# Kernel optimization log

Measured on AMD Instinct MI355X. Metric: run time of the kernel, lower is better.

The kernel has to match this reference:

```python
import jax, jax.numpy as jnp
import numpy as np

B, C, L = 2, 256, 2048   # batch, emb_dim, seq_len
D, H = 64, 8             # d_model (per-head), n_heads
HD = D * H
EPS = 1e-8


def glob_ln(x, gamma, beta):
    # x: (B, C, L); normalize over all non-batch dims, affine over channel dim 1
    mean = jnp.mean(x, axis=(1, 2), keepdims=True)
    var = jnp.mean((x - mean) ** 2, axis=(1, 2), keepdims=True)
    normed = (x - mean) / jnp.sqrt(var + EPS)
    return gamma[None, :, None] * normed + beta[None, :, None]


def pos_encoding(length, dim):
    pos = jnp.arange(length, dtype=jnp.float32)[:, None]
    div = jnp.exp(jnp.arange(0, dim, 2, dtype=jnp.float32) * (-np.log(10000.0) / dim))
    ang = pos * div  # (L, dim/2)
    return jnp.stack([jnp.sin(ang), jnp.cos(ang)], axis=-1).reshape(length, dim)


def setup_inputs() -> dict:
    key = jax.random.key(0)
    ks = jax.random.split(key, 16)
    s_in = 1.0 / np.sqrt(C)
    s_hd = 1.0 / np.sqrt(HD)
    return {
        "x": jax.random.normal(ks[0], (B, C, L), dtype=jnp.float32),
        "Wq": jax.random.uniform(ks[1], (HD, C), minval=-s_in, maxval=s_in),
        "bq": jax.random.uniform(ks[2], (HD,), minval=-s_in, maxval=s_in),
        "Wk": jax.random.uniform(ks[3], (HD, C), minval=-s_in, maxval=s_in),
        "bk": jax.random.uniform(ks[4], (HD,), minval=-s_in, maxval=s_in),
        "Wv": jax.random.uniform(ks[5], (HD, C), minval=-s_in, maxval=s_in),
        "bv": jax.random.uniform(ks[6], (HD,), minval=-s_in, maxval=s_in),
        "Wo": jax.random.uniform(ks[7], (C, HD), minval=-s_hd, maxval=s_hd),
        "bo": jax.random.uniform(ks[8], (C,), minval=-s_hd, maxval=s_hd),
        "g_mha": jnp.ones((C,)), "b_mha": jnp.zeros((C,)),
        "conv_w": jax.random.uniform(ks[9], (C, C), minval=-s_in, maxval=s_in),
        "conv_b": jax.random.uniform(ks[10], (C,), minval=-s_in, maxval=s_in),
        "g_ffn": jnp.ones((C,)), "b_ffn": jnp.zeros((C,)),
        "alpha": jnp.float32(0.25),
        "g_out": jnp.ones((C,)), "b_out": jnp.zeros((C,)),
    }


def reference(x, Wq, bq, Wk, bk, Wv, bv, Wo, bo, g_mha, b_mha,
              conv_w, conv_b, g_ffn, b_ffn, alpha, g_out, b_out):
    scale = 1.0 / np.sqrt(D)
    t = jnp.transpose(x, (0, 2, 1))            # (B, L, C)
    t = t + pos_encoding(L, C)[None]
    # multi-head attention (self)
    q = (scale * (t @ Wq.T + bq)).reshape(B, L, H, D)
    k = (t @ Wk.T + bk).reshape(B, L, H, D)
    v = (t @ Wv.T + bv).reshape(B, L, H, D)
    scores = jnp.einsum('nlhd,nshd->nhls', q, k)  # (B, H, L, L)
    attn = jax.nn.softmax(scores, axis=-1)
    o = jnp.einsum('nhls,nshd->nlhd', attn, v).reshape(B, L, HD)
    t = t + (o @ Wo.T + bo)                    # residual
    y = glob_ln(jnp.transpose(t, (0, 2, 1)), g_mha, b_mha)  # (B, C, L)
    # FFN: 1x1 conv + GlobLN + PReLU
    f = jnp.einsum('bcl,oc->bol', y, conv_w) + conv_b[None, :, None]
    f = glob_ln(f, g_ffn, b_ffn)
    f = jnp.where(f >= 0, f, alpha * f)
    return glob_ln(f + y, g_out, b_out)
```

## Files before the change

### kernel.cpp

```cpp
#include <hip/hip_runtime.h>
#include <hip/hip_bf16.h>
#include <math.h>

#define BB   2
#define CC   256
#define LL   2048
#define DD   64
#define HH   8
#define HDIM 512
#define BLQ  (BB*LL)
#define EPSV 1e-8f

typedef __attribute__((ext_vector_type(8))) short short8;
typedef __attribute__((ext_vector_type(4))) float f32x4;

__device__ __forceinline__ float wred_sum(float v) {
#pragma unroll
    for (int off = 32; off > 0; off >>= 1) v += __shfl_down(v, off, 64);
    return v;
}
__device__ __forceinline__ unsigned short f2bf(float x) {
    union { float f; unsigned u; } a; a.f = x;
    unsigned r = a.u + 0x7fff + ((a.u >> 16) & 1);
    return (unsigned short)(r >> 16);
}
__device__ __forceinline__ unsigned pk(float a, float b) {
    return (unsigned)f2bf(a) | ((unsigned)f2bf(b) << 16);
}
__device__ __forceinline__ short8 ld_frag(const unsigned short* p) {
    union { short8 v; uint2 u[2]; } f;
    f.u[0] = *(const uint2*)p;
    f.u[1] = *(const uint2*)(p + 4);
    return f.v;
}

__global__ __launch_bounds__(256) void k_prep(const float* __restrict__ x,
                                              float* __restrict__ t,
                                              unsigned short* __restrict__ tb) {
    __shared__ float tr[64][65];
    int l0 = blockIdx.x * 64, c0 = blockIdx.y * 64, b = blockIdx.z;
    int tid = threadIdx.x, r = tid >> 2, q = tid & 3;
#pragma unroll
    for (int p = 0; p < 4; ++p) {
        int lc = 4 * (q + 4 * p);
        float4 v = *(const float4*)&x[((size_t)(b * CC + c0 + r)) * LL + l0 + lc];
        tr[lc + 0][r] = v.x; tr[lc + 1][r] = v.y; tr[lc + 2][r] = v.z; tr[lc + 3][r] = v.w;
    }
    __syncthreads();
    int lg = l0 + r;
#pragma unroll
    for (int p = 0; p < 4; ++p) {
        int cc = 4 * (q + 4 * p);
        float4 v = *(const float4*)&tr[r][cc];
        float pe[4];
#pragma unroll
        for (int i = 0; i < 4; ++i) {
            int cg = c0 + cc + i;
            float freq = __expf((float)(cg & ~1) * (-9.210340371976184f / (float)CC));
            float ang = (float)lg * freq;
            pe[i] = (cg & 1) ? __cosf(ang) : __sinf(ang);
        }
        v.x += pe[0]; v.y += pe[1]; v.z += pe[2]; v.w += pe[3];
        size_t o = ((size_t)(b * LL + lg)) * CC + c0 + cc;
        *(float4*)&t[o] = v;
        uint2 u; u.x = pk(v.x, v.y); u.y = pk(v.z, v.w);
        *(uint2*)&tb[o] = u;
    }
}

__global__ __launch_bounds__(256) void k_cvtw(const float* __restrict__ Wq, const float* __restrict__ Wk,
                                              const float* __restrict__ Wv, const float* __restrict__ Wo,
                                              const float* __restrict__ Wc,
                                              unsigned short* __restrict__ dqkv,
                                              unsigned short* __restrict__ dWo,
                                              unsigned short* __restrict__ dWc) {
    int idx = (blockIdx.x * 256 + threadIdx.x) * 4;
    const float* s; unsigned short* d;
    if (idx < 131072)      { s = Wq + idx;          d = dqkv + idx; }
    else if (idx < 262144) { s = Wk + idx - 131072; d = dqkv + idx; }
    else if (idx < 393216) { s = Wv + idx - 262144; d = dqkv + idx; }
    else if (idx < 524288) { s = Wo + idx - 393216; d = dWo + idx - 393216; }
    else                   { s = Wc + idx - 524288; d = dWc + idx - 524288; }
    float4 v = *(const float4*)s;
    uint2 u; u.x = pk(v.x, v.y); u.y = pk(v.z, v.w);
    *(uint2*)d = u;
}

#define MLDK 68
__global__ __launch_bounds__(256) void k_mm(const unsigned short* __restrict__ A,
                                            const unsigned short* __restrict__ W,
                                            const float* __restrict__ b0,
                                            const float* __restrict__ b1,
                                            const float* __restrict__ b2,
                                            const float* resid,
                                            float* out, unsigned short* outb,
                                            float* pstat,
                                            int mode, int M, int N, int K) {
    __shared__ unsigned short As[2][64][MLDK];
    __shared__ unsigned short Ws[2][64][MLDK];
    __shared__ float rs[4][2];
    int tid = threadIdx.x;
    int w = tid >> 6, lane = tid & 63, g = lane >> 4, qi = lane & 15;
    int bm = blockIdx.x * 64, bn = blockIdx.y * 64;
    int wr = w >> 1, wc = w & 1;
    int srow = tid >> 2, sq = tid & 3;
    bool vseg = (mode == 1) && (bn >= 1024);
    f32x4 acc[2][2];
    acc[0][0] = acc[0][1] = acc[1][0] = acc[1][1] = (f32x4){0.f, 0.f, 0.f, 0.f};
    uint4 ra[2], rw[2];
#pragma unroll
    for (int p = 0; p < 2; ++p) {
        ra[p] = *(const uint4*)&A[(size_t)(bm + srow) * K + (sq + 4 * p) * 8];
        rw[p] = *(const uint4*)&W[(size_t)(bn + srow) * K + (sq + 4 * p) * 8];
    }
    int nt = K >> 6;
    for (int it = 0; it < nt; ++it) {
        int buf = it & 1;
#pragma unroll
        for (int p = 0; p < 2; ++p) {
            *(uint2*)&As[buf][srow][(sq + 4 * p) * 8]     = make_uint2(ra[p].x, ra[p].y);
            *(uint2*)&As[buf][srow][(sq + 4 * p) * 8 + 4] = make_uint2(ra[p].z, ra[p].w);
            *(uint2*)&Ws[buf][srow][(sq + 4 * p) * 8]     = make_uint2(rw[p].x, rw[p].y);
            *(uint2*)&Ws[buf][srow][(sq + 4 * p) * 8 + 4] = make_uint2(rw[p].z, rw[p].w);
        }
        __syncthreads();
        if (it + 1 < nt) {
            int k0 = (it + 1) << 6;
#pragma unroll
            for (int p = 0; p < 2; ++p) {
                ra[p] = *(const uint4*)&A[(size_t)(bm + srow) * K + k0 + (sq + 4 * p) * 8];
                rw[p] = *(const uint4*)&W[(size_t)(bn + srow) * K + k0 + (sq + 4 * p) * 8];
            }
        }
#pragma unroll
        for (int c = 0; c < 2; ++c) {
            short8 wf0 = ld_frag(&Ws[buf][wr * 32 + 0  + qi][c * 32 + 8 * g]);
            short8 wf1 = ld_frag(&Ws[buf][wr * 32 + 16 + qi][c * 32 + 8 * g]);
            short8 af0 = ld_frag(&As[buf][wc * 32 + 0  + qi][c * 32 + 8 * g]);
            short8 af1 = ld_frag(&As[buf][wc * 32 + 16 + qi][c * 32 + 8 * g]);
            if (!vseg) {
                acc[0][0] = __builtin_amdgcn_mfma_f32_16x16x32_bf16(wf0, af0, acc[0][0], 0, 0, 0);
                acc[0][1] = __builtin_amdgcn_mfma_f32_16x16x32_bf16(wf0, af1, acc[0][1], 0, 0, 0);
                acc[1][0] = __builtin_amdgcn_mfma_f32_16x16x32_bf16(wf1, af0, acc[1][0], 0, 0, 0);
                acc[1][1] = __builtin_amdgcn_mfma_f32_16x16x32_bf16(wf1, af1, acc[1][1], 0, 0, 0);
            } else {
                acc[0][0] = __builtin_amdgcn_mfma_f32_16x16x32_bf16(af0, wf0, acc[0][0], 0, 0, 0);
                acc[0][1] = __builtin_amdgcn_mfma_f32_16x16x32_bf16(af0, wf1, acc[0][1], 0, 0, 0);
                acc[1][0] = __builtin_amdgcn_mfma_f32_16x16x32_bf16(af1, wf0, acc[1][0], 0, 0, 0);
                acc[1][1] = __builtin_amdgcn_mfma_f32_16x16x32_bf16(af1, wf1, acc[1][1], 0, 0, 0);
            }
        }
    }
    if (mode == 0) {
        float s = 0.f, s2 = 0.f;
#pragma unroll
        for (int fi = 0; fi < 2; ++fi)
#pragma unroll
            for (int fj = 0; fj < 2; ++fj) {
                int n0 = bn + wr * 32 + fi * 16 + 4 * g;
                int m  = bm + wc * 32 + fj * 16 + qi;
                float4 bi = *(const float4*)&b0[n0];
                float4 v;
                v.x = acc[fi][fj][0] + bi.x; v.y = acc[fi][fj][1] + bi.y;
                v.z = acc[fi][fj][2] + bi.z; v.w = acc[fi][fj][3] + bi.w;
                if (resid) {
                    float4 rv = *(const float4*)&resid[(size_t)m * N + n0];
                    v.x += rv.x; v.y += rv.y; v.z += rv.z; v.w += rv.w;
                }
                *(float4*)&out[(size_t)m * N + n0] = v;
                s  += (v.x + v.y) + (v.z + v.w);
                s2 += v.x * v.x + v.y * v.y + v.z * v.z + v.w * v.w;
            }
        if (pstat) {
            s = wred_sum(s); s2 = wred_sum(s2);
            if (lane == 0) { rs[w][0] = s; rs[w][1] = s2; }
            __syncthreads();
            if (tid == 0) {
                int bid = blockIdx.y * gridDim.x + blockIdx.x;
                pstat[bid * 2 + 0] = rs[0][0] + rs[1][0] + rs[2][0] + rs[3][0];
                pstat[bid * 2 + 1] = rs[0][1] + rs[1][1] + rs[2][1] + rs[3][1];
            }
        }
    } else if (!vseg) {
        int seg = bn >> 9;
        const float* bs = seg ? b1 : b0;
        float sc = seg ? 1.f : 0.125f;
#pragma unroll
        for (int fi = 0; fi < 2; ++fi)
#pragma unroll
            for (int fj = 0; fj < 2; ++fj) {
                int nn0 = (bn & 511) + wr * 32 + fi * 16 + 4 * g;
                int m   = bm + wc * 32 + fj * 16 + qi;
                int b = m >> 11, l = m & (LL - 1);
                int h = nn0 >> 6, d0 = nn0 & 63;
                float4 bi = *(const float4*)&bs[nn0];
                uint2 u;
                u.x = pk(sc * (acc[fi][fj][0] + bi.x), sc * (acc[fi][fj][1] + bi.y));
                u.y = pk(sc * (acc[fi][fj][2] + bi.z), sc * (acc[fi][fj][3] + bi.w));
                *(uint2*)&outb[(size_t)seg * 2097152 +
                               (((size_t)(b * HH + h)) * LL + l) * DD + d0] = u;
            }
    } else {
#pragma unroll
        for (int fi = 0; fi < 2; ++fi)
#pragma unroll
            for (int fj = 0; fj < 2; ++fj) {
                int m0 = bm + wc * 32 + fi * 16 + 4 * g;
                int nn = (bn & 511) + wr * 32 + fj * 16 + qi;
                int b = m0 >> 11, l0 = m0 & (LL - 1);
                int h = nn >> 6, d = nn & 63;
                float bi = b2[nn];
                uint2 u;
                u.x = pk(acc[fi][fj][0] + bi, acc[fi][fj][1] + bi);
                u.y = pk(acc[fi][fj][2] + bi, acc[fi][fj][3] + bi);
                *(uint2*)&outb[(size_t)2 * 2097152 +
                               (((size_t)(b * HH + h)) * DD + d) * LL + l0] = u;
            }
    }
}

#define LDK 68
__global__ __launch_bounds__(256) void k_attn(const unsigned short* __restrict__ QKV,
                                              unsigned short* __restrict__ o) {
    int h = blockIdx.y, b = blockIdx.z;
    int tid = threadIdx.x;
    int w = tid >> 6, lane = tid & 63, g = lane >> 4, qi = lane & 15;
    int q0 = blockIdx.x * 64 + w * 16;
    __shared__ unsigned short Ks[2][64][LDK];
    __shared__ unsigned short Vts[2][64][LDK];
    __shared__ unsigned short Pw[4][16][LDK];
    const size_t bh = (size_t)(b * HH + h);
    const unsigned short* Qg = QKV + bh * LL * DD;
    const unsigned short* Kg = QKV + 2097152 + bh * LL * DD;
    const unsigned short* Vg = QKV + (size_t)2 * 2097152 + bh * DD * LL;

    short8 qf[2];
#pragma unroll
    for (int c = 0; c < 2; ++c)
        qf[c] = *(const short8*)&Qg[(size_t)(q0 + qi) * DD + c * 32 + 8 * g];

    f32x4 ot[4];
#pragma unroll
    for (int db = 0; db < 4; ++db) ot[db] = (f32x4){0.f, 0.f, 0.f, 0.f};
    float m = -INFINITY, sum = 0.f;

    int srow = tid >> 2, sq = tid & 3;
    uint4 kr[2], vr[2];
#pragma unroll
    for (int p = 0; p < 2; ++p) {
        kr[p] = *(const uint4*)&Kg[(size_t)srow * DD + (sq + 4 * p) * 8];
        vr[p] = *(const uint4*)&Vg[(size_t)srow * LL + (sq + 4 * p) * 8];
    }
    for (int it = 0; it < LL / 64; ++it) {
        int buf = it & 1;
#pragma unroll
        for (int p = 0; p < 2; ++p) {
            *(uint2*)&Ks[buf][srow][(sq + 4 * p) * 8]      = make_uint2(kr[p].x, kr[p].y);
            *(uint2*)&Ks[buf][srow][(sq + 4 * p) * 8 + 4]  = make_uint2(kr[p].z, kr[p].w);
            *(uint2*)&Vts[buf][srow][(sq + 4 * p) * 8]     = make_uint2(vr[p].x, vr[p].y);
            *(uint2*)&Vts[buf][srow][(sq + 4 * p) * 8 + 4] = make_uint2(vr[p].z, vr[p].w);
        }
        __syncthreads();
        if (it + 1 < LL / 64) {
            int s1 = (it + 1) * 64;
#pragma unroll
            for (int p = 0; p < 2; ++p) {
                kr[p] = *(const uint4*)&Kg[(size_t)(s1 + srow) * DD + (sq + 4 * p) * 8];
                vr[p] = *(const uint4*)&Vg[(size_t)srow * LL + s1 + (sq + 4 * p) * 8];
            }
        }
        f32x4 st[4];
        __builtin_amdgcn_s_setprio(1);
#pragma unroll
        for (int sb = 0; sb < 4; ++sb) {
            f32x4 a = (f32x4){0.f, 0.f, 0.f, 0.f};
#pragma unroll
            for (int c = 0; c < 2; ++c) {
                short8 kf = ld_frag(&Ks[buf][sb * 16 + qi][c * 32 + 8 * g]);
                a = __builtin_amdgcn_mfma_f32_16x16x32_bf16(kf, qf[c], a, 0, 0, 0);
            }
            st[sb] = a;
        }
        __builtin_amdgcn_s_setprio(0);
        float tmax = -INFINITY;
#pragma unroll
        for (int sb = 0; sb < 4; ++sb)
#pragma unroll
            for (int r = 0; r < 4; ++r) tmax = fmaxf(tmax, st[sb][r]);
        tmax = fmaxf(tmax, __shfl_xor(tmax, 16, 64));
        tmax = fmaxf(tmax, __shfl_xor(tmax, 32, 64));
        if (!__all(tmax - m <= 8.f)) {
            float mnew = fmaxf(m, tmax);
            float corr = __expf(m - mnew);
            m = mnew;
            sum *= corr;
#pragma unroll
            for (int db = 0; db < 4; ++db)
#pragma unroll
                for (int r = 0; r < 4; ++r) ot[db][r] *= corr;
        }
        float ps = 0.f;
#pragma unroll
        for (int sb = 0; sb < 4; ++sb) {
            float p0 = __expf(st[sb][0] - m);
            float p1 = __expf(st[sb][1] - m);
            float p2 = __expf(st[sb][2] - m);
            float p3 = __expf(st[sb][3] - m);
            ps += (p0 + p1) + (p2 + p3);
            uint2 w2; w2.x = pk(p0, p1); w2.y = pk(p2, p3);
            *(uint2*)&Pw[w][qi][sb * 16 + 4 * g] = w2;
        }
        sum += ps;
        __builtin_amdgcn_s_setprio(1);
#pragma unroll
        for (int db = 0; db < 4; ++db)
#pragma unroll
            for (int sc = 0; sc < 2; ++sc) {
                short8 vf = ld_frag(&Vts[buf][db * 16 + qi][sc * 32 + 8 * g]);
                short8 pf = ld_frag(&Pw[w][qi][sc * 32 + 8 * g]);
                ot[db] = __builtin_amdgcn_mfma_f32_16x16x32_bf16(vf, pf, ot[db], 0, 0, 0);
            }
        __builtin_amdgcn_s_setprio(0);
    }
    sum += __shfl_xor(sum, 16, 64);
    sum += __shfl_xor(sum, 32, 64);
    float rinv = 1.f / sum;
#pragma unroll
    for (int db = 0; db < 4; ++db) {
        int d0 = db * 16 + 4 * g;
        uint2 u;
        u.x = pk(ot[db][0] * rinv, ot[db][1] * rinv);
        u.y = pk(ot[db][2] * rinv, ot[db][3] * rinv);
        *(uint2*)&o[((size_t)(b * LL + q0 + qi)) * HDIM + h * DD + d0] = u;
    }
}

__global__ __launch_bounds__(256) void k_ln(const float* in,
                                            const float* __restrict__ g,
                                            const float* __restrict__ be,
                                            const float* __restrict__ pin,
                                            const float* __restrict__ add,
                                            const float* __restrict__ alpha_ptr,
                                            float* out, unsigned short* outb,
                                            float* pout) {
    __shared__ float rs[4][2];
    int tid = threadIdx.x;
    int b = blockIdx.x >> 9;
    float s = 0.f, s2 = 0.f;
    if (tid < 128) {
        int pidx = (tid >> 5) * 64 + b * 32 + (tid & 31);
        s  = pin[pidx * 2 + 0];
        s2 = pin[pidx * 2 + 1];
    }
    s = wred_sum(s); s2 = wred_sum(s2);
    if ((tid & 63) == 0 && tid < 128) { rs[tid >> 6][0] = s; rs[tid >> 6][1] = s2; }
    __syncthreads();
    float S = rs[0][0] + rs[1][0], S2 = rs[0][1] + rs[1][1];
    float mean = S / (float)(CC * LL);
    float inv  = rsqrtf(S2 / (float)(CC * LL) - mean * mean + EPSV);

    int idx = (blockIdx.x * 256 + tid) * 4;
    int c = idx & (CC - 1);
    float4 v  = *(const float4*)&in[idx];
    float4 gg = *(const float4*)&g[c];
    float4 bb = *(const float4*)&be[c];
    v.x = (v.x - mean) * inv * gg.x + bb.x;
    v.y = (v.y - mean) * inv * gg.y + bb.y;
    v.z = (v.z - mean) * inv * gg.z + bb.z;
    v.w = (v.w - mean) * inv * gg.w + bb.w;
    if (alpha_ptr) {
        float al = alpha_ptr[0];
        v.x = v.x >= 0.f ? v.x : al * v.x;
        v.y = v.y >= 0.f ? v.y : al * v.y;
        v.z = v.z >= 0.f ? v.z : al * v.z;
        v.w = v.w >= 0.f ? v.w : al * v.w;
    }
    if (add) {
        float4 a = *(const float4*)&add[idx];
        v.x += a.x; v.y += a.y; v.z += a.z; v.w += a.w;
    }
    *(float4*)&out[idx] = v;
    if (outb) {
        uint2 u; u.x = pk(v.x, v.y); u.y = pk(v.z, v.w);
        *(uint2*)&outb[idx] = u;
    }
    if (pout) {
        float os  = (v.x + v.y) + (v.z + v.w);
        float os2 = v.x * v.x + v.y * v.y + v.z * v.z + v.w * v.w;
        os = wred_sum(os); os2 = wred_sum(os2);
        __syncthreads();
        if ((tid & 63) == 0) { rs[tid >> 6][0] = os; rs[tid >> 6][1] = os2; }
        __syncthreads();
        if (tid == 0) {
            pout[blockIdx.x * 2 + 0] = rs[0][0] + rs[1][0] + rs[2][0] + rs[3][0];
            pout[blockIdx.x * 2 + 1] = rs[0][1] + rs[1][1] + rs[2][1] + rs[3][1];
        }
    }
}

__global__ __launch_bounds__(256) void k_ln_t(const float* __restrict__ in,
                                              const float* __restrict__ g,
                                              const float* __restrict__ be,
                                              const float* __restrict__ pin,
                                              float* __restrict__ out) {
    __shared__ float tr[64][65];
    __shared__ float rs[4][2];
    int l0 = blockIdx.x * 64, c0 = blockIdx.y * 64, b = blockIdx.z;
    int tid = threadIdx.x, r = tid >> 2, q = tid & 3;
    float s  = pin[(b * 512 + tid) * 2 + 0] + pin[(b * 512 + 256 + tid) * 2 + 0];
    float s2 = pin[(b * 512 + tid) * 2 + 1] + pin[(b * 512 + 256 + tid) * 2 + 1];
    s = wred_sum(s); s2 = wred_sum(s2);
    if ((tid & 63) == 0) { rs[tid >> 6][0] = s; rs[tid >> 6][1] = s2; }
    __syncthreads();
    float S = rs[0][0] + rs[1][0] + rs[2][0] + rs[3][0];
    float S2 = rs[0][1] + rs[1][1] + rs[2][1] + rs[3][1];
    float mean = S / (float)(CC * LL);
    float inv  = rsqrtf(S2 / (float)(CC * LL) - mean * mean + EPSV);
#pragma unroll
    for (int p = 0; p < 4; ++p) {
        int cc = 4 * (q + 4 * p);
        float4 v  = *(const float4*)&in[((size_t)(b * LL + l0 + r)) * CC + c0 + cc];
        float4 gg = *(const float4*)&g[c0 + cc];
        float4 bb = *(const float4*)&be[c0 + cc];
        tr[cc + 0][r] = (v.x - mean) * inv * gg.x + bb.x;
        tr[cc + 1][r] = (v.y - mean) * inv * gg.y + bb.y;
        tr[cc + 2][r] = (v.z - mean) * inv * gg.z + bb.z;
        tr[cc + 3][r] = (v.w - mean) * inv * gg.w + bb.w;
    }
    __syncthreads();
#pragma unroll
    for (int p = 0; p < 4; ++p) {
        int ll = 4 * (q + 4 * p);
        float4 v = *(const float4*)&tr[r][ll];
        *(float4*)&out[((size_t)(b * CC + c0 + r)) * LL + l0 + ll] = v;
    }
}

extern "C" void kernel_launch(void* const* d_in, const int* in_sizes, int n_in,
                              void* d_out, int out_size, void* d_ws, size_t ws_size,
                              hipStream_t stream) {
    const float* x      = (const float*)d_in[0];
    const float* Wq     = (const float*)d_in[1];
    const float* bq     = (const float*)d_in[2];
    const float* Wk     = (const float*)d_in[3];
    const float* bk     = (const float*)d_in[4];
    const float* Wv     = (const float*)d_in[5];
    const float* bv     = (const float*)d_in[6];
    const float* Wo     = (const float*)d_in[7];
    const float* bo     = (const float*)d_in[8];
    const float* g_mha  = (const float*)d_in[9];
    const float* b_mha  = (const float*)d_in[10];
    const float* conv_w = (const float*)d_in[11];
    const float* conv_b = (const float*)d_in[12];
    const float* g_ffn  = (const float*)d_in[13];
    const float* b_ffn  = (const float*)d_in[14];
    const float* alpha  = (const float*)d_in[15];
    const float* g_out  = (const float*)d_in[16];
    const float* b_out  = (const float*)d_in[17];
    float* out = (float*)d_out;

    float* ws = (float*)d_ws;
    float* t             = ws;
    unsigned short* tb   = (unsigned short*)(ws + 1048576);
    unsigned short* QKVb = (unsigned short*)(ws + 1572864);
    float* f             = ws + 1572864;
    unsigned short* ybf  = (unsigned short*)(ws + 2621440);
    unsigned short* obuf = (unsigned short*)(ws + 4718592);
    unsigned short* Wqkvb= (unsigned short*)(ws + 5767168);
    unsigned short* Wob  = (unsigned short*)(ws + 5963776);
    unsigned short* Wcb  = (unsigned short*)(ws + 6029312);
    float* pstatA        = ws + 6062080;
    float* pstatB        = ws + 6062592;
    float* pstatC        = ws + 6063104;

    dim3 gtile(LL / 64, CC / 64, BB);
    k_prep<<<gtile, 256, 0, stream>>>(x, t, tb);
    k_cvtw<<<576, 256, 0, stream>>>(Wq, Wk, Wv, Wo, conv_w, Wqkvb, Wob, Wcb);

    dim3 gqkv(BLQ / 64, 1536 / 64);
    k_mm<<<gqkv, 256, 0, stream>>>(tb, Wqkvb, bq, bk, bv, nullptr, nullptr, QKVb,
                                   nullptr, 1, BLQ, 1536, CC);

    dim3 gattn(LL / 64, HH, BB);
    k_attn<<<gattn, 256, 0, stream>>>(QKVb, obuf);

    dim3 go(BLQ / 64, CC / 64);
    k_mm<<<go, 256, 0, stream>>>(obuf, Wob, bo, nullptr, nullptr, t, t, nullptr,
                                 pstatA, 0, BLQ, CC, HDIM);

    k_ln<<<1024, 256, 0, stream>>>(t, g_mha, b_mha, pstatA, nullptr, nullptr,
                                   t, ybf, nullptr);

    k_mm<<<go, 256, 0, stream>>>(ybf, Wcb, conv_b, nullptr, nullptr, nullptr, f, nullptr,
                                 pstatB, 0, BLQ, CC, CC);

    k_ln<<<1024, 256, 0, stream>>>(f, g_ffn, b_ffn, pstatB, t, alpha,
                                   f, nullptr, pstatC);

    k_ln_t<<<gtile, 256, 0, stream>>>(f, g_out, b_out, pstatC, out);
}
```

Measured before the change: 95.41 us.

## Merge weight conversion into prep kernel, use exp2 softmax and MFMA row sums

Folds the weight bf16 conversion kernel into the prep kernel through a flattened grid, which removes one launch. Folds log2(e) into the Q scale so the attention softmax uses exp2f instead of __expf. The running row sum is now computed with an extra MFMA against a ones vector, which removes the per-lane scalar sums and the shuffle reduction but adds one more MFMA and accumulator per tile. It also swaps the hand-written bf16 rounding for the HIP intrinsic. The sum comes from bf16-rounded probabilities, so normalization changes slightly.

Result: no change. 96.31 us (+0.9%).

```diff
diff --git a/kernel.cpp b/kernel.cpp
--- a/kernel.cpp
+++ b/kernel.cpp
@@ -10,6 +10,7 @@
 #define HDIM 512
 #define BLQ  (BB*LL)
 #define EPSV 1e-8f
+#define QSCALE (0.125f * 1.44269504088896f)
 
 typedef __attribute__((ext_vector_type(8))) short short8;
 typedef __attribute__((ext_vector_type(4))) float f32x4;
@@ -19,13 +20,10 @@
     for (int off = 32; off > 0; off >>= 1) v += __shfl_down(v, off, 64);
     return v;
 }
-__device__ __forceinline__ unsigned short f2bf(float x) {
-    union { float f; unsigned u; } a; a.f = x;
-    unsigned r = a.u + 0x7fff + ((a.u >> 16) & 1);
-    return (unsigned short)(r >> 16);
-}
 __device__ __forceinline__ unsigned pk(float a, float b) {
-    return (unsigned)f2bf(a) | ((unsigned)f2bf(b) << 16);
+    __hip_bfloat162 h = __float22bfloat162_rn(make_float2(a, b));
+    union { __hip_bfloat162 h; unsigned u; } c; c.h = h;
+    return c.u;
 }
 __device__ __forceinline__ short8 ld_frag(const unsigned short* p) {
     union { short8 v; uint2 u[2]; } f;
@@ -35,11 +33,32 @@
 }
 
 __global__ __launch_bounds__(256) void k_prep(const float* __restrict__ x,
+                                              const float* __restrict__ Wq, const float* __restrict__ Wk,
+                                              const float* __restrict__ Wv, const float* __restrict__ Wo,
+                                              const float* __restrict__ Wc,
                                               float* __restrict__ t,
-                                              unsigned short* __restrict__ tb) {
+                                              unsigned short* __restrict__ tb,
+                                              unsigned short* __restrict__ dqkv,
+                                              unsigned short* __restrict__ dWo,
+                                              unsigned short* __restrict__ dWc) {
+    int bid = blockIdx.x;
+    int tid = threadIdx.x;
+    if (bid >= 256) {
+        int idx = ((bid - 256) * 256 + tid) * 4;
+        const float* s; unsigned short* d;
+        if (idx < 131072)      { s = Wq + idx;          d = dqkv + idx; }
+        else if (idx < 262144) { s = Wk + idx - 131072; d = dqkv + idx; }
+        else if (idx < 393216) { s = Wv + idx - 262144; d = dqkv + idx; }
+        else if (idx < 524288) { s = Wo + idx - 393216; d = dWo + idx - 393216; }
+        else                   { s = Wc + idx - 524288; d = dWc + idx - 524288; }
+        float4 v = *(const float4*)s;
+        uint2 u; u.x = pk(v.x, v.y); u.y = pk(v.z, v.w);
+        *(uint2*)d = u;
+        return;
+    }
     __shared__ float tr[64][65];
-    int l0 = blockIdx.x * 64, c0 = blockIdx.y * 64, b = blockIdx.z;
-    int tid = threadIdx.x, r = tid >> 2, q = tid & 3;
+    int l0 = (bid & 31) * 64, c0 = ((bid >> 5) & 3) * 64, b = bid >> 7;
+    int r = tid >> 2, q = tid & 3;
 #pragma unroll
     for (int p = 0; p < 4; ++p) {
         int lc = 4 * (q + 4 * p);
@@ -66,24 +85,6 @@
         uint2 u; u.x = pk(v.x, v.y); u.y = pk(v.z, v.w);
         *(uint2*)&tb[o] = u;
     }
-}
-
-__global__ __launch_bounds__(256) void k_cvtw(const float* __restrict__ Wq, const float* __restrict__ Wk,
-                                              const float* __restrict__ Wv, const float* __restrict__ Wo,
-                                              const float* __restrict__ Wc,
-                                              unsigned short* __restrict__ dqkv,
-                                              unsigned short* __restrict__ dWo,
-                                              unsigned short* __restrict__ dWc) {
-    int idx = (blockIdx.x * 256 + threadIdx.x) * 4;
-    const float* s; unsigned short* d;
-    if (idx < 131072)      { s = Wq + idx;          d = dqkv + idx; }
-    else if (idx < 262144) { s = Wk + idx - 131072; d = dqkv + idx; }
-    else if (idx < 393216) { s = Wv + idx - 262144; d = dqkv + idx; }
-    else if (idx < 524288) { s = Wo + idx - 393216; d = dWo + idx - 393216; }
-    else                   { s = Wc + idx - 524288; d = dWc + idx - 524288; }
-    float4 v = *(const float4*)s;
-    uint2 u; u.x = pk(v.x, v.y); u.y = pk(v.z, v.w);
-    *(uint2*)d = u;
 }
 
 #define MLDK 68
@@ -184,7 +185,7 @@
     } else if (!vseg) {
         int seg = bn >> 9;
         const float* bs = seg ? b1 : b0;
-        float sc = seg ? 1.f : 0.125f;
+        float sc = seg ? 1.f : QSCALE;
 #pragma unroll
         for (int fi = 0; fi < 2; ++fi)
 #pragma unroll
@@ -238,11 +239,14 @@
 #pragma unroll
     for (int c = 0; c < 2; ++c)
         qf[c] = *(const short8*)&Qg[(size_t)(q0 + qi) * DD + c * 32 + 8 * g];
-
-    f32x4 ot[4];
-#pragma unroll
-    for (int db = 0; db < 4; ++db) ot[db] = (f32x4){0.f, 0.f, 0.f, 0.f};
-    float m = -INFINITY, sum = 0.f;
+    short8 ones;
+#pragma unroll
+    for (int i = 0; i < 8; ++i) ones[i] = (short)0x3F80;
+
+    f32x4 ot[5];
+#pragma unroll
+    for (int db = 0; db < 5; ++db) ot[db] = (f32x4){0.f, 0.f, 0.f, 0.f};
+    float m = -INFINITY;
 
     int srow = tid >> 2, sq = tid & 3;
     uint4 kr[2], vr[2];
@@ -282,49 +286,45 @@
             st[sb] = a;
         }
         __builtin_amdgcn_s_setprio(0);
-        float tmax = -INFINITY;
-#pragma unroll
-        for (int sb = 0; sb < 4; ++sb)
-#pragma unroll
-            for (int r = 0; r < 4; ++r) tmax = fmaxf(tmax, st[sb][r]);
+        float t0 = fmaxf(fmaxf(st[0][0], st[0][1]), fmaxf(st[0][2], st[0][3]));
+        float t1 = fmaxf(fmaxf(st[1][0], st[1][1]), fmaxf(st[1][2], st[1][3]));
+        float t2 = fmaxf(fmaxf(st[2][0], st[2][1]), fmaxf(st[2][2], st[2][3]));
+        float t3 = fmaxf(fmaxf(st[3][0], st[3][1]), fmaxf(st[3][2], st[3][3]));
+        float tmax = fmaxf(fmaxf(t0, t1), fmaxf(t2, t3));
         tmax = fmaxf(tmax, __shfl_xor(tmax, 16, 64));
         tmax = fmaxf(tmax, __shfl_xor(tmax, 32, 64));
         if (!__all(tmax - m <= 8.f)) {
             float mnew = fmaxf(m, tmax);
-            float corr = __expf(m - mnew);
+            float corr = exp2f(m - mnew);
             m = mnew;
-            sum *= corr;
-#pragma unroll
-            for (int db = 0; db < 4; ++db)
+#pragma unroll
+            for (int db = 0; db < 5; ++db)
 #pragma unroll
                 for (int r = 0; r < 4; ++r) ot[db][r] *= corr;
         }
-        float ps = 0.f;
 #pragma unroll
         for (int sb = 0; sb < 4; ++sb) {
-            float p0 = __expf(st[sb][0] - m);
-            float p1 = __expf(st[sb][1] - m);
-            float p2 = __expf(st[sb][2] - m);
-            float p3 = __expf(st[sb][3] - m);
-            ps += (p0 + p1) + (p2 + p3);
+            float p0 = exp2f(st[sb][0] - m);
+            float p1 = exp2f(st[sb][1] - m);
+            float p2 = exp2f(st[sb][2] - m);
+            float p3 = exp2f(st[sb][3] - m);
             uint2 w2; w2.x = pk(p0, p1); w2.y = pk(p2, p3);
             *(uint2*)&Pw[w][qi][sb * 16 + 4 * g] = w2;
         }
-        sum += ps;
         __builtin_amdgcn_s_setprio(1);
 #pragma unroll
-        for (int db = 0; db < 4; ++db)
-#pragma unroll
-            for (int sc = 0; sc < 2; ++sc) {
+        for (int sc = 0; sc < 2; ++sc) {
+            short8 pf = ld_frag(&Pw[w][qi][sc * 32 + 8 * g]);
+            ot[4] = __builtin_amdgcn_mfma_f32_16x16x32_bf16(ones, pf, ot[4], 0, 0, 0);
+#pragma unroll
+            for (int db = 0; db < 4; ++db) {
                 short8 vf = ld_frag(&Vts[buf][db * 16 + qi][sc * 32 + 8 * g]);
-                short8 pf = ld_frag(&Pw[w][qi][sc * 32 + 8 * g]);
                 ot[db] = __builtin_amdgcn_mfma_f32_16x16x32_bf16(vf, pf, ot[db], 0, 0, 0);
             }
+        }
         __builtin_amdgcn_s_setprio(0);
     }
-    sum += __shfl_xor(sum, 16, 64);
-    sum += __shfl_xor(sum, 32, 64);
-    float rinv = 1.f / sum;
+    float rinv = 1.f / ot[4][0];
 #pragma unroll
     for (int db = 0; db < 4; ++db) {
         int d0 = db * 16 + 4 * g;
@@ -473,9 +473,7 @@
     float* pstatB        = ws + 6062592;
     float* pstatC        = ws + 6063104;
 
-    dim3 gtile(LL / 64, CC / 64, BB);
-    k_prep<<<gtile, 256, 0, stream>>>(x, t, tb);
-    k_cvtw<<<576, 256, 0, stream>>>(Wq, Wk, Wv, Wo, conv_w, Wqkvb, Wob, Wcb);
+    k_prep<<<832, 256, 0, stream>>>(x, Wq, Wk, Wv, Wo, conv_w, t, tb, Wqkvb, Wob, Wcb);
 
     dim3 gqkv(BLQ / 64, 1536 / 64);
     k_mm<<<gqkv, 256, 0, stream>>>(tb, Wqkvb, bq, bk, bv, nullptr, nullptr, QKVb,
@@ -497,5 +495,5 @@
     k_ln<<<1024, 256, 0, stream>>>(f, g_ffn, b_ffn, pstatB, t, alpha,
                                    f, nullptr, pstatC);
 
-    k_ln_t<<<gtile, 256, 0, stream>>>(f, g_out, b_out, pstatC, out);
-}
+    k_ln_t<<<dim3(LL / 64, CC / 64, BB), 256, 0, stream>>>(f, g_out, b_out, pstatC, out);
+}
```
